# Optimization experiments

Hardware: AMD Instinct MI355X
Metric: run time of the kernel (lower is better)

## Reference

```python
import jax, jax.numpy as jnp
import numpy as np

NUM_LOCAL = 4      # num_local_experts
E_TOTAL = 8        # local + unpopular experts
HIDDEN = 1024
FFN = 4 * HIDDEN
CAP = 2048         # tokens (capacity) per expert
D0 = 1             # leading dim of inputs / output_tensor


def setup_inputs() -> dict:
    key = jax.random.key(0)
    k_in, k_w0, k_w3 = jax.random.split(key, 3)
    inputs = jax.random.normal(k_in, (D0, E_TOTAL, CAP, HIDDEN), dtype=jnp.float32)
    # gating-activity indicator per expert; all-ones -> all unpopular experts active
    output_tensor = jnp.ones((D0, E_TOTAL), dtype=jnp.float32)
    # stacked per-expert MLP weights (torch Linear convention: [out, in])
    w0 = jax.random.normal(k_w0, (E_TOTAL, FFN, HIDDEN), dtype=jnp.float32) * 0.02
    w3 = jax.random.normal(k_w3, (E_TOTAL, HIDDEN, FFN), dtype=jnp.float32) * 0.02
    return {"output_tensor": output_tensor, "inputs": inputs, "w0": w0, "w3": w3}


def reference(output_tensor, inputs, w0, w3):
    # Grouped 2-layer MLP per expert: x @ w0^T -> GELU -> @ w3^T
    # b: D0, e: expert, c: capacity, d: hidden, f: ffn
    h = jnp.einsum('becd,efd->becf', inputs, w0)
    h = jax.nn.gelu(h, approximate=False)  # torch nn.GELU default = exact erf
    out = jnp.einsum('becf,edf->becd', h, w3)
    # unpopular experts with zero activity produce zeros (scatter-into-zeros combine)
    unpop_mask = jnp.sum(output_tensor[:, NUM_LOCAL:], axis=0) != 0  # [E_unpop]
    full_mask = jnp.concatenate(
        [jnp.ones((NUM_LOCAL,), dtype=bool), unpop_mask])  # locals always computed
    out = out * full_mask[None, :, None, None].astype(out.dtype)
    return out
```

## Files before the change

kernel.cpp:

```cpp
#include <hip/hip_runtime.h>
#include <math.h>

#define E_TOTAL 8
#define NUM_LOCAL 4
#define HIDDEN 1024
#define FFN 4096
#define CAP 2048

typedef unsigned short ushort_t;
typedef __attribute__((ext_vector_type(8))) short short8;
typedef __attribute__((ext_vector_type(8))) unsigned short u16x8;
typedef __attribute__((ext_vector_type(4))) float f32x4;

__device__ __forceinline__ unsigned short f2bf(float f) {
  unsigned int u = __float_as_uint(f);
  u += 0x7FFFu + ((u >> 16) & 1u);
  return (unsigned short)(u >> 16);
}

__device__ __forceinline__ void gload_lds16(const void* g, void* l) {
  __builtin_amdgcn_global_load_lds(
      (const __attribute__((address_space(1))) void*)g,
      (__attribute__((address_space(3))) void*)l,
      16, 0, 0);
}

__device__ __forceinline__ float fast_gelu(float v) {
  const float x = v * 0.70710678118654752f;
  const float ax = fabsf(x);
  const float t = 1.f / (1.f + 0.3275911f * ax);
  const float p =
      t * (0.254829592f +
           t * (-0.284496736f +
                t * (1.421413741f + t * (-1.453152027f + t * 1.061405429f))));
  float erfv = 1.f - p * __expf(-ax * ax);
  erfv = copysignf(erfv, x);
  return 0.5f * v * (1.f + erfv);
}

__global__ __launch_bounds__(256) void cvt_kernel(const float4* __restrict__ s,
                                                  u16x8* __restrict__ d) {
  const size_t i = (size_t)blockIdx.x * 256 + threadIdx.x;
  float4 a = s[2 * i], b = s[2 * i + 1];
  u16x8 o;
  o[0] = f2bf(a.x); o[1] = f2bf(a.y); o[2] = f2bf(a.z); o[3] = f2bf(a.w);
  o[4] = f2bf(b.x); o[5] = f2bf(b.y); o[6] = f2bf(b.z); o[7] = f2bf(b.w);
  d[i] = o;
}

template <int KD>
__device__ __forceinline__ void stage_half(const ushort_t* g, char* dst,
                                           int tid) {
  gload_lds16(g, dst + tid * 16);
  gload_lds16(g + (size_t)64 * KD, dst + 8192 + tid * 16);
}

#define LOAD_A4(F0)                                                          \
  do {                                                                       \
    _Pragma("unroll") for (int ks = 0; ks < 2; ++ks)                         \
    _Pragma("unroll") for (int i = 0; i < 4; ++i)                            \
      af[i][ks] = *(const short8*)(sAc + aoff[ks] + ((F0) + i) * 2048);      \
  } while (0)

#define LOAD_B2(J0)                                                          \
  do {                                                                       \
    _Pragma("unroll") for (int ks = 0; ks < 2; ++ks)                         \
    _Pragma("unroll") for (int j = 0; j < 2; ++j)                            \
      bf[(J0) + j][ks] =                                                     \
          *(const short8*)(sBc + boff[ks] + ((J0) + j) * 2048);              \
  } while (0)

#define MFMA16(MI0, NJ0)                                                     \
  do {                                                                       \
    __builtin_amdgcn_s_setprio(1);                                           \
    _Pragma("unroll") for (int ks = 0; ks < 2; ++ks)                         \
    _Pragma("unroll") for (int i = 0; i < 4; ++i)                            \
    _Pragma("unroll") for (int j = 0; j < 2; ++j)                            \
      acc[(MI0) + i][(NJ0) + j] = __builtin_amdgcn_mfma_f32_16x16x32_bf16(   \
          af[i][ks], bf[(NJ0) + j][ks], acc[(MI0) + i][(NJ0) + j], 0, 0, 0); \
    __builtin_amdgcn_s_setprio(0);                                           \
  } while (0)

#define PHASE_SYNC()                                                         \
  __builtin_amdgcn_s_barrier();                                              \
  asm volatile("s_waitcnt lgkmcnt(0)" ::: "memory");                         \
  __builtin_amdgcn_sched_barrier(0)

template <int M, int N, int K, bool GELU_OUT>
__global__ __launch_bounds__(512, 2) void gemm_nt8(
    const ushort_t* __restrict__ A, const ushort_t* __restrict__ B,
    void* __restrict__ Cout, const float* __restrict__ ot, int d0) {
  __shared__ char sA[2][32768];
  __shared__ char sB[2][32768];
  constexpr int NT = K / 64;
  static_assert(NT >= 2, "pipeline needs >=2 K-tiles");

  const int e = blockIdx.z;
  const int bm = blockIdx.x * 256;
  const int bn = blockIdx.y * 256;
  const int tid = threadIdx.x;
  const int lane = tid & 63, wv = tid >> 6;
  const int wr = wv >> 2, wc = wv & 3;
  const int quad = lane >> 4, l16 = lane & 15;
  const int swz = l16 & 7;

  const int rp = tid >> 3;
  const int cs = (tid & 7) ^ (rp & 7);
  const ushort_t* gA = A + (size_t)e * M * K + (size_t)(bm + rp) * K + cs * 8;
  const ushort_t* gB = B + (size_t)e * N * K + (size_t)(bn + rp) * K + cs * 8;

  int aoff[2], boff[2];
#pragma unroll
  for (int ks = 0; ks < 2; ++ks) {
    aoff[ks] = (wr * 128 + l16) * 128 + (((ks * 4 + quad) ^ swz) << 4);
    boff[ks] = (wc * 64 + l16) * 128 + (((ks * 4 + quad) ^ swz) << 4);
  }

  f32x4 acc[8][4];
#pragma unroll
  for (int i = 0; i < 8; ++i)
#pragma unroll
    for (int j = 0; j < 4; ++j) {
      f32x4 z = {0.f, 0.f, 0.f, 0.f};
      acc[i][j] = z;
    }

  short8 af[4][2];
  short8 bf[4][2];

  stage_half<K>(gA, sA[0], tid);
  stage_half<K>(gA + (size_t)128 * K, sA[0] + 16384, tid);
  stage_half<K>(gB, sB[0], tid);
  stage_half<K>(gB + (size_t)128 * K, sB[0] + 16384, tid);
  stage_half<K>(gB + 64, sB[1], tid);
  stage_half<K>(gB + (size_t)128 * K + 64, sB[1] + 16384, tid);
  asm volatile("s_waitcnt vmcnt(4)" ::: "memory");
  __builtin_amdgcn_sched_barrier(0);
  __builtin_amdgcn_s_barrier();

#pragma unroll 2
  for (int t = 0; t < NT; ++t) {
    char* sAc = sA[t & 1];
    char* sBc = sB[t & 1];
    char* sAn = sA[(t + 1) & 1];
    const size_t ko1 = (size_t)(t + 1) * 64;
    const size_t ko2 = (size_t)(t + 2) * 64;

    LOAD_A4(0);
    LOAD_B2(0);
    if (t + 1 < NT) stage_half<K>(gA + ko1, sAn, tid);
    PHASE_SYNC();
    MFMA16(0, 0);
    __builtin_amdgcn_s_barrier();

    LOAD_B2(2);
    if (t + 1 < NT) stage_half<K>(gA + (size_t)128 * K + ko1, sAn + 16384, tid);
    PHASE_SYNC();
    MFMA16(0, 2);
    __builtin_amdgcn_s_barrier();

    LOAD_A4(4);
    if (t + 2 < NT) stage_half<K>(gB + ko2, sBc, tid);
    PHASE_SYNC();
    MFMA16(4, 0);
    __builtin_amdgcn_s_barrier();

    if (t + 2 < NT) stage_half<K>(gB + (size_t)128 * K + ko2, sBc + 16384, tid);
    PHASE_SYNC();
    MFMA16(4, 2);
    if (t + 2 < NT) {
      asm volatile("s_waitcnt vmcnt(4)" ::: "memory");
    } else {
      asm volatile("s_waitcnt vmcnt(0)" ::: "memory");
    }
    __builtin_amdgcn_sched_barrier(0);
    __builtin_amdgcn_s_barrier();
  }

  if (GELU_OUT) {
    ushort_t* C = (ushort_t*)Cout + (size_t)e * M * N +
                  (size_t)(bm + wr * 128) * N + (bn + wc * 64);
#pragma unroll
    for (int mi = 0; mi < 8; ++mi)
#pragma unroll
      for (int r = 0; r < 4; ++r) {
        const int row = mi * 16 + quad * 4 + r;
#pragma unroll
        for (int ni = 0; ni < 4; ++ni)
          C[(size_t)row * N + ni * 16 + l16] = f2bf(fast_gelu(acc[mi][ni][r]));
      }
  } else {
    float mask = 1.f;
    if (e >= NUM_LOCAL) {
      float s = 0.f;
      for (int b = 0; b < d0; ++b) s += ot[b * E_TOTAL + e];
      mask = (s != 0.f) ? 1.f : 0.f;
    }
    float* C = (float*)Cout + (size_t)e * M * N +
               (size_t)(bm + wr * 128) * N + (bn + wc * 64);
#pragma unroll
    for (int mi = 0; mi < 8; ++mi)
#pragma unroll
      for (int r = 0; r < 4; ++r) {
        const int row = mi * 16 + quad * 4 + r;
#pragma unroll
        for (int ni = 0; ni < 4; ++ni)
          C[(size_t)row * N + ni * 16 + l16] = acc[mi][ni][r] * mask;
      }
  }
}

extern "C" void kernel_launch(void* const* d_in, const int* in_sizes, int n_in,
                              void* d_out, int out_size, void* d_ws,
                              size_t ws_size, hipStream_t stream) {
  const float* ot = (const float*)d_in[0];
  const float* x  = (const float*)d_in[1];
  const float* w0 = (const float*)d_in[2];
  const float* w3 = (const float*)d_in[3];
  const int d0 = in_sizes[0] / E_TOTAL;

  char* ws = (char*)d_ws;
  ushort_t* xb  = (ushort_t*)ws;
  ushort_t* w0b = (ushort_t*)(ws + (size_t)32 * 1024 * 1024);
  ushort_t* w3b = (ushort_t*)ws;
  ushort_t* h   = (ushort_t*)(ws + (size_t)96 * 1024 * 1024);

  const int nx = E_TOTAL * CAP * HIDDEN;
  const int nw = E_TOTAL * FFN * HIDDEN;

  cvt_kernel<<<nx / (256 * 8), 256, 0, stream>>>((const float4*)x, (u16x8*)xb);
  cvt_kernel<<<nw / (256 * 8), 256, 0, stream>>>((const float4*)w0, (u16x8*)w0b);

  gemm_nt8<CAP, FFN, HIDDEN, true>
      <<<dim3(CAP / 256, FFN / 256, E_TOTAL), 512, 0, stream>>>(
          xb, w0b, h, nullptr, d0);

  cvt_kernel<<<nw / (256 * 8), 256, 0, stream>>>((const float4*)w3, (u16x8*)w3b);

  gemm_nt8<CAP, HIDDEN, FFN, false>
      <<<dim3(CAP / 256, HIDDEN / 256, E_TOTAL), 512, 0, stream>>>(
          h, w3b, d_out, ot, d0);
}
```

Baseline: 646.8 us.

## Use 128x128 single-buffered GEMM for first layer and add XCD block swizzle

New measurement: 632.0 us. -2.3%, faster.

```diff
diff --git a/kernel.cpp b/kernel.cpp
--- a/kernel.cpp
+++ b/kernel.cpp
@@ -48,6 +48,107 @@
   d[i] = o;
 }
 
+template <int M, int N, int K, bool GELU_OUT>
+__global__ __launch_bounds__(256, 2) void gemm_nt(
+    const ushort_t* __restrict__ A, const ushort_t* __restrict__ B,
+    void* __restrict__ Cout, const float* __restrict__ ot, int d0) {
+  __shared__ ushort_t lds_a[128 * 64];
+  __shared__ ushort_t lds_b[128 * 64];
+
+  constexpr int GX = M / 128, GY = N / 128;
+  constexpr int NWG = GX * GY * E_TOTAL;
+  static_assert(NWG % 8 == 0, "bijective swizzle needs nwg%8==0");
+  int dfl = blockIdx.x + GX * (blockIdx.y + GY * blockIdx.z);
+  dfl = (dfl & 7) * (NWG / 8) + (dfl >> 3);
+  const int e = dfl / (GX * GY);
+  const int rem = dfl % (GX * GY);
+  const int bm = (rem % GX) * 128;
+  const int bn = (rem / GX) * 128;
+
+  const int t = threadIdx.x;
+  const int wave = t >> 6, lane = t & 63;
+  const int wr = wave >> 1, wc = wave & 1;
+  const int quad = lane >> 4, l16 = lane & 15;
+  const int r8 = lane >> 3;
+  const int s8 = lane & 7;
+  const int g8 = (s8 + r8) & 7;
+
+  const ushort_t* Ag = A + (size_t)e * M * K + (size_t)(bm + r8) * K + g8 * 8;
+  const ushort_t* Bg = B + (size_t)e * N * K + (size_t)(bn + r8) * K + g8 * 8;
+
+  f32x4 acc[4][4];
+#pragma unroll
+  for (int i = 0; i < 4; ++i)
+#pragma unroll
+    for (int j = 0; j < 4; ++j) {
+      f32x4 z = {0.f, 0.f, 0.f, 0.f};
+      acc[i][j] = z;
+    }
+
+  for (int kb = 0; kb < K / 64; ++kb) {
+    const size_t ko = (size_t)kb * 64;
+#pragma unroll
+    for (int j = 0; j < 4; ++j) {
+      const int R = (j * 4 + wave) * 8;
+      gload_lds16(Ag + ko + (size_t)R * K, &lds_a[R * 64]);
+      gload_lds16(Bg + ko + (size_t)R * K, &lds_b[R * 64]);
+    }
+    __syncthreads();
+
+#pragma unroll
+    for (int ks = 0; ks < 2; ++ks) {
+      short8 af[4], bfr[4];
+      const int c = ks * 4 + quad;
+#pragma unroll
+      for (int i = 0; i < 4; ++i) {
+        const int ra = wr * 64 + i * 16 + l16;
+        const int rb = wc * 64 + i * 16 + l16;
+        af[i]  = *(const short8*)&lds_a[ra * 64 + ((c - ra) & 7) * 8];
+        bfr[i] = *(const short8*)&lds_b[rb * 64 + ((c - rb) & 7) * 8];
+      }
+#pragma unroll
+      for (int mi = 0; mi < 4; ++mi)
+#pragma unroll
+        for (int ni = 0; ni < 4; ++ni)
+          acc[mi][ni] = __builtin_amdgcn_mfma_f32_16x16x32_bf16(
+              af[mi], bfr[ni], acc[mi][ni], 0, 0, 0);
+    }
+    __syncthreads();
+  }
+
+  if (GELU_OUT) {
+    ushort_t* C = (ushort_t*)Cout + (size_t)e * M * N +
+                  (size_t)(bm + wr * 64) * N + (bn + wc * 64);
+#pragma unroll
+    for (int mi = 0; mi < 4; ++mi)
+#pragma unroll
+      for (int r = 0; r < 4; ++r) {
+        const int row = mi * 16 + quad * 4 + r;
+#pragma unroll
+        for (int ni = 0; ni < 4; ++ni)
+          C[(size_t)row * N + ni * 16 + l16] = f2bf(fast_gelu(acc[mi][ni][r]));
+      }
+  } else {
+    float mask = 1.f;
+    if (e >= NUM_LOCAL) {
+      float s = 0.f;
+      for (int b = 0; b < d0; ++b) s += ot[b * E_TOTAL + e];
+      mask = (s != 0.f) ? 1.f : 0.f;
+    }
+    float* C = (float*)Cout + (size_t)e * M * N +
+               (size_t)(bm + wr * 64) * N + (bn + wc * 64);
+#pragma unroll
+    for (int mi = 0; mi < 4; ++mi)
+#pragma unroll
+      for (int r = 0; r < 4; ++r) {
+        const int row = mi * 16 + quad * 4 + r;
+#pragma unroll
+        for (int ni = 0; ni < 4; ++ni)
+          C[(size_t)row * N + ni * 16 + l16] = acc[mi][ni][r] * mask;
+      }
+  }
+}
+
 template <int KD>
 __device__ __forceinline__ void stage_half(const ushort_t* g, char* dst,
                                            int tid) {
@@ -95,9 +196,16 @@
   constexpr int NT = K / 64;
   static_assert(NT >= 2, "pipeline needs >=2 K-tiles");
 
-  const int e = blockIdx.z;
-  const int bm = blockIdx.x * 256;
-  const int bn = blockIdx.y * 256;
+  constexpr int GX = M / 256, GY = N / 256;
+  constexpr int NWG = GX * GY * E_TOTAL;
+  static_assert(NWG % 8 == 0, "bijective swizzle needs nwg%8==0");
+  int dfl = blockIdx.x + GX * (blockIdx.y + GY * blockIdx.z);
+  dfl = (dfl & 7) * (NWG / 8) + (dfl >> 3);
+  const int e = dfl / (GX * GY);
+  const int rem = dfl % (GX * GY);
+  const int bm = (rem % GX) * 256;
+  const int bn = (rem / GX) * 256;
+
   const int tid = threadIdx.x;
   const int lane = tid & 63, wv = tid >> 6;
   const int wr = wv >> 2, wc = wv & 3;
@@ -231,8 +339,8 @@
   cvt_kernel<<<nx / (256 * 8), 256, 0, stream>>>((const float4*)x, (u16x8*)xb);
   cvt_kernel<<<nw / (256 * 8), 256, 0, stream>>>((const float4*)w0, (u16x8*)w0b);
 
-  gemm_nt8<CAP, FFN, HIDDEN, true>
-      <<<dim3(CAP / 256, FFN / 256, E_TOTAL), 512, 0, stream>>>(
+  gemm_nt<CAP, FFN, HIDDEN, true>
+      <<<dim3(CAP / 128, FFN / 128, E_TOTAL), 256, 0, stream>>>(
           xb, w0b, h, nullptr, d0);
 
   cvt_kernel<<<nw / (256 * 8), 256, 0, stream>>>((const float4*)w3, (u16x8*)w3b);
```
